# Kernel optimization log

Hardware: AMD Instinct MI355X
Metric: run time of the kernel (lower is better)

The kernel has to match this reference:

```python
import jax, jax.numpy as jnp
import numpy as np

EPS = 1e-5


def setup_inputs() -> dict:
    key = jax.random.key(0)
    ks = jax.random.split(key, 5)
    N, E, D, L = 10000, 160000, 512, 3
    x = jax.random.normal(ks[0], (N, D), dtype=jnp.float32)
    src = jax.random.randint(ks[1], (E,), 0, N, dtype=jnp.int64)
    dst = jax.random.randint(ks[2], (E,), 0, N, dtype=jnp.int64)
    gamma = jnp.ones((L, D), dtype=jnp.float32)
    beta = jnp.zeros((L, D), dtype=jnp.float32)
    # glorot-ish scale so ReLU stack stays well-conditioned
    W = jax.random.normal(ks[3], (L, D, D), dtype=jnp.float32) * (1.0 / np.sqrt(D))
    b = jnp.zeros((L, D), dtype=jnp.float32)
    return {"x": x, "src": src, "dst": dst, "gamma": gamma, "beta": beta, "W": W, "b": b}


def reference(x, src, dst, gamma, beta, W, b):
    N = x.shape[0]
    ones = jnp.ones(src.shape[0], dtype=x.dtype)
    # DGL GraphConv norm='both': src side uses out-degree, dst side uses in-degree
    out_deg = jnp.clip(jax.ops.segment_sum(ones, src, num_segments=N), 1.0)
    in_deg = jnp.clip(jax.ops.segment_sum(ones, dst, num_segments=N), 1.0)
    src_norm = (out_deg ** -0.5)[:, None]  # [N,1]
    dst_norm = (in_deg ** -0.5)[:, None]   # [N,1]
    n_layers = gamma.shape[0]
    for i in range(n_layers):
        # BatchNorm1d (training mode: batch mean, biased variance)
        mu = jnp.mean(x, axis=0)
        var = jnp.var(x, axis=0)
        x = (x - mu) * jax.lax.rsqrt(var + EPS) * gamma[i] + beta[i]
        h = x * src_norm
        agg = jax.ops.segment_sum(h[src], dst, num_segments=N) * dst_norm
        x = jax.nn.relu(agg @ W[i] + b[i])
    return x
```

## Files before the change

kernel.cpp:

```cpp
#include <hip/hip_runtime.h>
#include <hip/hip_bf16.h>

constexpr int N = 10000;
constexpr int D = 512;
constexpr int E = 160000;
constexpr int L = 3;
constexpr float EPS = 1e-5f;

typedef _Float16 half8 __attribute__((ext_vector_type(8)));
typedef _Float16 half2v __attribute__((ext_vector_type(2)));
typedef float floatx4 __attribute__((ext_vector_type(4)));

__device__ __forceinline__ void glds16(const _Float16* g, _Float16* l) {
    __builtin_amdgcn_global_load_lds(
        (const __attribute__((address_space(1))) uint32_t*)(g),
        (__attribute__((address_space(3))) uint32_t*)(l),
        16, 0, 0);
}

constexpr int DEG_BLOCKS  = (E + 255) / 256;
constexpr int CONV_BLOCKS = 100;
constexpr int TW_BLOCKS   = L * 256;
constexpr int MEGA_BLOCKS = DEG_BLOCKS + CONV_BLOCKS + TW_BLOCKS;

__global__ __launch_bounds__(256) void mega_setup(
    const int* __restrict__ src, const int* __restrict__ dst,
    const float* __restrict__ x, const float* __restrict__ W,
    int* __restrict__ out_deg, int* __restrict__ in_deg,
    _Float16* __restrict__ x16, float* __restrict__ stats0,
    _Float16* __restrict__ Wt) {
    __shared__ float tb[32][33];
    int bid = blockIdx.x;
    int tid = threadIdx.x;
    if (bid < DEG_BLOCKS) {
        int e = bid * 256 + tid;
        if (e < E) {
            atomicAdd(&out_deg[src[e]], 1);
            atomicAdd(&in_deg[dst[e]], 1);
        }
    } else if (bid < DEG_BLOCKS + CONV_BLOCKS) {
        int b = bid - DEG_BLOCKS;
        int r0 = b * 100;
        int r1 = r0 + 100; if (r1 > N) r1 = N;
        int c2 = tid * 2;
        float s0 = 0.f, s1 = 0.f, q0 = 0.f, q1 = 0.f;
        for (int r = r0; r < r1; ++r) {
            float2 v = *(const float2*)(x + (size_t)r * D + c2);
            s0 += v.x; q0 += v.x * v.x;
            s1 += v.y; q1 += v.y * v.y;
            half2v h; h[0] = (_Float16)v.x; h[1] = (_Float16)v.y;
            *(half2v*)(x16 + (size_t)r * D + c2) = h;
        }
        atomicAdd(&stats0[c2], s0);
        atomicAdd(&stats0[c2 + 1], s1);
        atomicAdd(&stats0[D + c2], q0);
        atomicAdd(&stats0[D + c2 + 1], q1);
    } else {
        int b = bid - DEG_BLOCKS - CONV_BLOCKS;
        int l = b >> 8;
        int t = b & 255;
        int k0 = (t >> 4) * 32, n0 = (t & 15) * 32;
        int tx = tid & 31, ty = tid >> 5;
        const float* Wl = W + (size_t)l * D * D;
        _Float16* Wtl = Wt + (size_t)l * D * D;
        for (int i = 0; i < 32; i += 8)
            tb[ty + i][tx] = Wl[(size_t)(k0 + ty + i) * D + n0 + tx];
        __syncthreads();
        for (int i = 0; i < 32; i += 8)
            Wtl[(size_t)(n0 + ty + i) * D + k0 + tx] = (_Float16)tb[tx][ty + i];
    }
}

__global__ void scan_indeg(const int* __restrict__ in_deg,
                           const int* __restrict__ out_deg,
                           int* __restrict__ off, int* __restrict__ cursor,
                           float* __restrict__ src_norm, float* __restrict__ dst_norm) {
    __shared__ int lsum[1024];
    int t = threadIdx.x;
    const int chunk = (N + 1023) / 1024;
    int start = t * chunk;
    int end = start + chunk; if (end > N) end = N;
    int s = 0;
    for (int i = start; i < end; ++i) s += in_deg[i];
    lsum[t] = s;
    __syncthreads();
    for (int d = 1; d < 1024; d <<= 1) {
        int v = (t >= d) ? lsum[t - d] : 0;
        __syncthreads();
        lsum[t] += v;
        __syncthreads();
    }
    int excl = (t == 0) ? 0 : lsum[t - 1];
    for (int i = start; i < end; ++i) {
        off[i] = excl;
        cursor[i] = excl;
        excl += in_deg[i];
        int od = out_deg[i]; if (od < 1) od = 1;
        int id = in_deg[i];  if (id < 1) id = 1;
        src_norm[i] = rsqrtf((float)od);
        dst_norm[i] = rsqrtf((float)id);
    }
    if (t == 1023) off[N] = lsum[1023];
}

__global__ void csr_fill(const int* __restrict__ src, const int* __restrict__ dst,
                         int* __restrict__ cursor, int* __restrict__ csr_src) {
    int e = blockIdx.x * blockDim.x + threadIdx.x;
    if (e >= E) return;
    int d = dst[e];
    int pos = atomicAdd(&cursor[d], 1);
    csr_src[pos] = src[e];
}

__global__ __launch_bounds__(256) void aggregate_bn(
    const _Float16* __restrict__ x, const int* __restrict__ off,
    const int* __restrict__ csr_src, const float* __restrict__ src_norm,
    const float* __restrict__ dst_norm, const float* __restrict__ stats,
    const float* __restrict__ gamma, const float* __restrict__ beta,
    _Float16* __restrict__ agg) {
    int wid = (blockIdx.x * 256 + threadIdx.x) >> 6;
    if (wid >= N) return;
    int lane = threadIdx.x & 63;
    int c0 = lane * 8;

    float scale[8], shift[8];
    const float invN = 1.0f / (float)N;
    for (int i = 0; i < 8; ++i) {
        int c = c0 + i;
        float mu = stats[c] * invN;
        float var = stats[D + c] * invN - mu * mu;
        float sc = gamma[c] * rsqrtf(var + EPS);
        scale[i] = sc;
        shift[i] = beta[c] - mu * sc;
    }

    int e0 = off[wid], e1 = off[wid + 1];
    float a[8] = {}, a2[8] = {};
    float t = 0.f;
    int e = e0;
    for (; e + 4 <= e1; e += 4) {
        int s0 = csr_src[e];
        int s1 = csr_src[e + 1];
        int s2 = csr_src[e + 2];
        int s3 = csr_src[e + 3];
        float n0 = src_norm[s0];
        float n1 = src_norm[s1];
        float n2 = src_norm[s2];
        float n3 = src_norm[s3];
        half8 v0 = *(const half8*)(x + (size_t)s0 * D + c0);
        half8 v1 = *(const half8*)(x + (size_t)s1 * D + c0);
        half8 v2 = *(const half8*)(x + (size_t)s2 * D + c0);
        half8 v3 = *(const half8*)(x + (size_t)s3 * D + c0);
        t += (n0 + n1) + (n2 + n3);
        for (int k = 0; k < 8; ++k) {
            a[k]  += (float)v0[k] * n0;
            a2[k] += (float)v1[k] * n1;
            a[k]  += (float)v2[k] * n2;
            a2[k] += (float)v3[k] * n3;
        }
    }
    for (; e < e1; ++e) {
        int s0 = csr_src[e];
        float n0 = src_norm[s0];
        half8 v0 = *(const half8*)(x + (size_t)s0 * D + c0);
        t += n0;
        for (int k = 0; k < 8; ++k) a[k] += (float)v0[k] * n0;
    }
    float dn = dst_norm[wid];
    half8 o;
    for (int i = 0; i < 8; ++i)
        o[i] = (_Float16)(dn * (scale[i] * (a[i] + a2[i]) + shift[i] * t));
    *(half8*)(agg + (size_t)wid * D + c0) = o;
}

template <typename OutT, bool STATS>
__global__ __launch_bounds__(256) void mm_f16_relu(
    const _Float16* __restrict__ A, const _Float16* __restrict__ Bt,
    const float* __restrict__ bias, OutT* __restrict__ C, int M,
    float* __restrict__ stats) {
    __shared__ __align__(16) _Float16 As[128 * 32];
    __shared__ __align__(16) _Float16 Bs[128 * 32];
    const int tid  = threadIdx.x;
    const int wave = tid >> 6;
    const int lane = tid & 63;
    const int quad = lane >> 4;
    const int l16  = lane & 15;
    const int row0 = blockIdx.x * 128;
    const int col0 = blockIdx.y * 128;
    const int wm = (wave & 1) * 64;
    const int wn = (wave >> 1) * 64;
    const int sr = lane >> 2;
    const int sc = (lane & 3) * 8;

    int ar0 = row0 + wave * 32 + sr;
    int ar1 = ar0 + 16;
    if (ar0 >= M) ar0 = M - 1;
    if (ar1 >= M) ar1 = M - 1;
    const _Float16* gA0 = A + (size_t)ar0 * D + sc;
    const _Float16* gA1 = A + (size_t)ar1 * D + sc;
    const _Float16* gB0 = Bt + (size_t)(col0 + wave * 32 + sr) * D + sc;
    const _Float16* gB1 = Bt + (size_t)(col0 + wave * 32 + 16 + sr) * D + sc;
    _Float16* lA0 = As + (wave * 32) * 32;
    _Float16* lA1 = As + (wave * 32 + 16) * 32;
    _Float16* lB0 = Bs + (wave * 32) * 32;
    _Float16* lB1 = Bs + (wave * 32 + 16) * 32;

    floatx4 acc[4][4] = {};

    for (int k0 = 0; k0 < D; k0 += 32) {
        __syncthreads();
        glds16(gA0 + k0, lA0);
        glds16(gA1 + k0, lA1);
        glds16(gB0 + k0, lB0);
        glds16(gB1 + k0, lB1);
        __syncthreads();
        half8 af[4], bf[4];
        for (int i = 0; i < 4; ++i)
            af[i] = *(const half8*)(As + (wm + i * 16 + l16) * 32 + quad * 8);
        for (int j = 0; j < 4; ++j)
            bf[j] = *(const half8*)(Bs + (wn + j * 16 + l16) * 32 + quad * 8);
        for (int i = 0; i < 4; ++i)
            for (int j = 0; j < 4; ++j)
                acc[i][j] = __builtin_amdgcn_mfma_f32_16x16x32_f16(
                    af[i], bf[j], acc[i][j], 0, 0, 0);
    }

    float s[4] = {}, q[4] = {};
    for (int i = 0; i < 4; ++i) {
        for (int r = 0; r < 4; ++r) {
            int row = row0 + wm + i * 16 + quad * 4 + r;
            bool valid = row < M;
            for (int j = 0; j < 4; ++j) {
                int col = col0 + wn + j * 16 + l16;
                float v = acc[i][j][r] + bias[col];
                v = v > 0.f ? v : 0.f;
                if (valid) {
                    C[(size_t)row * D + col] = (OutT)v;
                    if (STATS) { s[j] += v; q[j] += v * v; }
                }
            }
        }
    }
    if (STATS) {
        for (int j = 0; j < 4; ++j) {
            float sv = s[j], qv = q[j];
            sv += __shfl_xor(sv, 16); sv += __shfl_xor(sv, 32);
            qv += __shfl_xor(qv, 16); qv += __shfl_xor(qv, 32);
            if (quad == 0) {
                int col = col0 + wn + j * 16 + l16;
                atomicAdd(&stats[col], sv);
                atomicAdd(&stats[D + col], qv);
            }
        }
    }
}

extern "C" void kernel_launch(void* const* d_in, const int* in_sizes, int n_in,
                              void* d_out, int out_size, void* d_ws, size_t ws_size,
                              hipStream_t stream) {
    const float* x_in  = (const float*)d_in[0];
    const int*   src   = (const int*)d_in[1];
    const int*   dst   = (const int*)d_in[2];
    const float* gamma = (const float*)d_in[3];
    const float* beta  = (const float*)d_in[4];
    const float* W     = (const float*)d_in[5];
    const float* b     = (const float*)d_in[6];
    float* out = (float*)d_out;

    char* p = (char*)d_ws;
    _Float16* x16 = (_Float16*)p;  p += (size_t)N * D * 2;
    _Float16* agg = (_Float16*)p;  p += (size_t)N * D * 2;
    _Float16* Wt  = (_Float16*)p;  p += (size_t)L * D * D * 2;
    float* src_norm = (float*)p;   p += (size_t)N * 4;
    float* dst_norm = (float*)p;   p += (size_t)N * 4;
    int* out_deg   = (int*)p;      p += (size_t)N * 4;
    int* in_deg    = (int*)p;      p += (size_t)N * 4;
    float* stats0  = (float*)p;    p += 2 * D * 4;
    float* stats1  = (float*)p;    p += 2 * D * 4;
    float* stats2  = (float*)p;    p += 2 * D * 4;
    int* csr_off   = (int*)p;      p += (size_t)(N + 1) * 4;
    int* cursor    = (int*)p;      p += (size_t)N * 4;
    int* csr_src   = (int*)p;      p += (size_t)E * 4;

    float* stats_in[3] = {stats0, stats1, stats2};

    hipMemsetAsync(out_deg, 0, (2 * (size_t)N + 6 * D) * sizeof(int), stream);
    mega_setup<<<MEGA_BLOCKS, 256, 0, stream>>>(src, dst, x_in, W,
                                                out_deg, in_deg, x16, stats0, Wt);
    scan_indeg<<<1, 1024, 0, stream>>>(in_deg, out_deg, csr_off, cursor,
                                       src_norm, dst_norm);
    csr_fill<<<DEG_BLOCKS, 256, 0, stream>>>(src, dst, cursor, csr_src);

    dim3 mm_grid((N + 127) / 128, D / 128);
    const int agg_blocks = (N + 3) / 4;

    for (int l = 0; l < L; ++l) {
        const float* gl  = gamma + (size_t)l * D;
        const float* bl  = beta + (size_t)l * D;
        const _Float16* Wl = Wt + (size_t)l * D * D;
        const float* bil = b + (size_t)l * D;

        aggregate_bn<<<agg_blocks, 256, 0, stream>>>(
            x16, csr_off, csr_src, src_norm, dst_norm, stats_in[l], gl, bl, agg);
        if (l == L - 1) {
            mm_f16_relu<float, false><<<mm_grid, 256, 0, stream>>>(
                agg, Wl, bil, out, N, nullptr);
        } else {
            mm_f16_relu<_Float16, true><<<mm_grid, 256, 0, stream>>>(
                agg, Wl, bil, x16, N, stats_in[l + 1]);
        }
    }
}
```

Before: 281.4 us.

## Store activations in column-chunked layout to shrink gather working set

Feature activations and aggregation outputs are stored as four column chunks of 128 halves each ([chunk][N][128]) instead of row-major [N][512]. The aggregation kernel now assigns each block to one chunk and eight nodes, so concurrently running blocks gather from a smaller slice of memory that fits better in cache. Each lane now reads 4-byte half2 values instead of 16-byte half8 values, which means more, narrower gathers and repeated index and norm loads per chunk. The GEMM A loads and the layer-output stores are updated to use the chunked layout.

```diff
diff --git a/kernel.cpp b/kernel.cpp
--- a/kernel.cpp
+++ b/kernel.cpp
@@ -6,6 +6,8 @@
 constexpr int E = 160000;
 constexpr int L = 3;
 constexpr float EPS = 1e-5f;
+constexpr int CHUNK = 128;
+constexpr int NCH = D / CHUNK;
 
 typedef _Float16 half8 __attribute__((ext_vector_type(8)));
 typedef _Float16 half2v __attribute__((ext_vector_type(2)));
@@ -43,13 +45,16 @@
         int r0 = b * 100;
         int r1 = r0 + 100; if (r1 > N) r1 = N;
         int c2 = tid * 2;
+        int ch = c2 >> 7;
+        int lc = c2 & 127;
+        _Float16* xc = x16 + (size_t)ch * N * CHUNK;
         float s0 = 0.f, s1 = 0.f, q0 = 0.f, q1 = 0.f;
         for (int r = r0; r < r1; ++r) {
             float2 v = *(const float2*)(x + (size_t)r * D + c2);
             s0 += v.x; q0 += v.x * v.x;
             s1 += v.y; q1 += v.y * v.y;
             half2v h; h[0] = (_Float16)v.x; h[1] = (_Float16)v.y;
-            *(half2v*)(x16 + (size_t)r * D + c2) = h;
+            *(half2v*)(xc + (size_t)r * CHUNK + lc) = h;
         }
         atomicAdd(&stats0[c2], s0);
         atomicAdd(&stats0[c2 + 1], s1);
@@ -118,15 +123,24 @@
     const float* __restrict__ dst_norm, const float* __restrict__ stats,
     const float* __restrict__ gamma, const float* __restrict__ beta,
     _Float16* __restrict__ agg) {
-    int wid = (blockIdx.x * 256 + threadIdx.x) >> 6;
-    if (wid >= N) return;
+    int bid = blockIdx.x;
+    int g = bid >> 3;
+    int xx = bid & 7;
+    int ch = xx >> 1;
+    int sub = xx & 1;
+    int wave = threadIdx.x >> 6;
     int lane = threadIdx.x & 63;
-    int c0 = lane * 8;
-
-    float scale[8], shift[8];
+    int n = g * 8 + sub * 4 + wave;
+    int lc = lane * 2;
+    int gc = ch * CHUNK + lc;
+
+    const _Float16* xc = x + (size_t)ch * N * CHUNK;
+    _Float16* ac = agg + (size_t)ch * N * CHUNK;
+
+    float scale[2], shift[2];
     const float invN = 1.0f / (float)N;
-    for (int i = 0; i < 8; ++i) {
-        int c = c0 + i;
+    for (int i = 0; i < 2; ++i) {
+        int c = gc + i;
         float mu = stats[c] * invN;
         float var = stats[D + c] * invN - mu * mu;
         float sc = gamma[c] * rsqrtf(var + EPS);
@@ -134,8 +148,8 @@
         shift[i] = beta[c] - mu * sc;
     }
 
-    int e0 = off[wid], e1 = off[wid + 1];
-    float a[8] = {}, a2[8] = {};
+    int e0 = off[n], e1 = off[n + 1];
+    float a[2] = {}, a2[2] = {};
     float t = 0.f;
     int e = e0;
     for (; e + 4 <= e1; e += 4) {
@@ -147,30 +161,28 @@
         float n1 = src_norm[s1];
         float n2 = src_norm[s2];
         float n3 = src_norm[s3];
-        half8 v0 = *(const half8*)(x + (size_t)s0 * D + c0);
-        half8 v1 = *(const half8*)(x + (size_t)s1 * D + c0);
-        half8 v2 = *(const half8*)(x + (size_t)s2 * D + c0);
-        half8 v3 = *(const half8*)(x + (size_t)s3 * D + c0);
+        half2v v0 = *(const half2v*)(xc + (size_t)s0 * CHUNK + lc);
+        half2v v1 = *(const half2v*)(xc + (size_t)s1 * CHUNK + lc);
+        half2v v2 = *(const half2v*)(xc + (size_t)s2 * CHUNK + lc);
+        half2v v3 = *(const half2v*)(xc + (size_t)s3 * CHUNK + lc);
         t += (n0 + n1) + (n2 + n3);
-        for (int k = 0; k < 8; ++k) {
-            a[k]  += (float)v0[k] * n0;
-            a2[k] += (float)v1[k] * n1;
-            a[k]  += (float)v2[k] * n2;
-            a2[k] += (float)v3[k] * n3;
+        for (int k = 0; k < 2; ++k) {
+            a[k]  += (float)v0[k] * n0 + (float)v2[k] * n2;
+            a2[k] += (float)v1[k] * n1 + (float)v3[k] * n3;
         }
     }
     for (; e < e1; ++e) {
         int s0 = csr_src[e];
         float n0 = src_norm[s0];
-        half8 v0 = *(const half8*)(x + (size_t)s0 * D + c0);
+        half2v v0 = *(const half2v*)(xc + (size_t)s0 * CHUNK + lc);
         t += n0;
-        for (int k = 0; k < 8; ++k) a[k] += (float)v0[k] * n0;
-    }
-    float dn = dst_norm[wid];
-    half8 o;
-    for (int i = 0; i < 8; ++i)
+        for (int k = 0; k < 2; ++k) a[k] += (float)v0[k] * n0;
+    }
+    float dn = dst_norm[n];
+    half2v o;
+    for (int i = 0; i < 2; ++i)
         o[i] = (_Float16)(dn * (scale[i] * (a[i] + a2[i]) + shift[i] * t));
-    *(half8*)(agg + (size_t)wid * D + c0) = o;
+    *(half2v*)(ac + (size_t)n * CHUNK + lc) = o;
 }
 
 template <typename OutT, bool STATS>
@@ -196,8 +208,8 @@
     int ar1 = ar0 + 16;
     if (ar0 >= M) ar0 = M - 1;
     if (ar1 >= M) ar1 = M - 1;
-    const _Float16* gA0 = A + (size_t)ar0 * D + sc;
-    const _Float16* gA1 = A + (size_t)ar1 * D + sc;
+    const size_t aoff0 = (size_t)ar0 * CHUNK + sc;
+    const size_t aoff1 = (size_t)ar1 * CHUNK + sc;
     const _Float16* gB0 = Bt + (size_t)(col0 + wave * 32 + sr) * D + sc;
     const _Float16* gB1 = Bt + (size_t)(col0 + wave * 32 + 16 + sr) * D + sc;
     _Float16* lA0 = As + (wave * 32) * 32;
@@ -208,9 +220,10 @@
     floatx4 acc[4][4] = {};
 
     for (int k0 = 0; k0 < D; k0 += 32) {
-        __syncthreads();
-        glds16(gA0 + k0, lA0);
-        glds16(gA1 + k0, lA1);
+        const _Float16* Ac = A + (size_t)(k0 >> 7) * M * CHUNK + (k0 & 127);
+        __syncthreads();
+        glds16(Ac + aoff0, lA0);
+        glds16(Ac + aoff1, lA1);
         glds16(gB0 + k0, lB0);
         glds16(gB1 + k0, lB1);
         __syncthreads();
@@ -225,18 +238,23 @@
                     af[i], bf[j], acc[i][j], 0, 0, 0);
     }
 
+    _Float16* Cc = (_Float16*)C + (size_t)(col0 >> 7) * M * CHUNK;
     float s[4] = {}, q[4] = {};
     for (int i = 0; i < 4; ++i) {
         for (int r = 0; r < 4; ++r) {
             int row = row0 + wm + i * 16 + quad * 4 + r;
             bool valid = row < M;
             for (int j = 0; j < 4; ++j) {
-                int col = col0 + wn + j * 16 + l16;
-                float v = acc[i][j][r] + bias[col];
+                int lcol = wn + j * 16 + l16;
+                float v = acc[i][j][r] + bias[col0 + lcol];
                 v = v > 0.f ? v : 0.f;
                 if (valid) {
-                    C[(size_t)row * D + col] = (OutT)v;
-                    if (STATS) { s[j] += v; q[j] += v * v; }
+                    if (STATS) {
+                        Cc[(size_t)row * CHUNK + lcol] = (_Float16)v;
+                        s[j] += v; q[j] += v * v;
+                    } else {
+                        C[(size_t)row * D + col0 + lcol] = (OutT)v;
+                    }
                 }
             }
         }
@@ -292,7 +310,7 @@
     csr_fill<<<DEG_BLOCKS, 256, 0, stream>>>(src, dst, cursor, csr_src);
 
     dim3 mm_grid((N + 127) / 128, D / 128);
-    const int agg_blocks = (N + 3) / 4;
+    const int agg_blocks = (N / 8) * 8;
 
     for (int l = 0; l < L; ++l) {
         const float* gl  = gamma + (size_t)l * D;
```

After: 296.6 us. +5.4%, slower.

## Split node features into two column-chunk planes for cache-friendlier gather

Applied to the files above, without the earlier changes.

Stores the fp16 node features as two planes of 256 columns each ([2][N][256]) instead of row-major [N][512]. The aggregation kernel runs twice as many blocks, each covering one column half with 4-wide loads, so each plane (about 5 MB) is more likely to stay in cache during the random neighbor gather. The GEMM epilogue and the setup conversion write into the chunked layout. In exchange, index and CSR loads are repeated per chunk and vector loads get narrower.

```diff
diff --git a/kernel.cpp b/kernel.cpp
--- a/kernel.cpp
+++ b/kernel.cpp
@@ -6,8 +6,10 @@
 constexpr int E = 160000;
 constexpr int L = 3;
 constexpr float EPS = 1e-5f;
+constexpr int CH = 256;
 
 typedef _Float16 half8 __attribute__((ext_vector_type(8)));
+typedef _Float16 half4v __attribute__((ext_vector_type(4)));
 typedef _Float16 half2v __attribute__((ext_vector_type(2)));
 typedef float floatx4 __attribute__((ext_vector_type(4)));
 
@@ -43,13 +45,16 @@
         int r0 = b * 100;
         int r1 = r0 + 100; if (r1 > N) r1 = N;
         int c2 = tid * 2;
+        int ch = c2 >> 8;
+        int lc = c2 & 255;
+        _Float16* xc = x16 + (size_t)ch * N * CH;
         float s0 = 0.f, s1 = 0.f, q0 = 0.f, q1 = 0.f;
         for (int r = r0; r < r1; ++r) {
             float2 v = *(const float2*)(x + (size_t)r * D + c2);
             s0 += v.x; q0 += v.x * v.x;
             s1 += v.y; q1 += v.y * v.y;
             half2v h; h[0] = (_Float16)v.x; h[1] = (_Float16)v.y;
-            *(half2v*)(x16 + (size_t)r * D + c2) = h;
+            *(half2v*)(xc + (size_t)r * CH + lc) = h;
         }
         atomicAdd(&stats0[c2], s0);
         atomicAdd(&stats0[c2 + 1], s1);
@@ -118,15 +123,21 @@
     const float* __restrict__ dst_norm, const float* __restrict__ stats,
     const float* __restrict__ gamma, const float* __restrict__ beta,
     _Float16* __restrict__ agg) {
-    int wid = (blockIdx.x * 256 + threadIdx.x) >> 6;
-    if (wid >= N) return;
+    int bid = blockIdx.x;
+    int ch = bid >= 2500;
+    int bb = ch ? bid - 2500 : bid;
+    int wave = threadIdx.x >> 6;
     int lane = threadIdx.x & 63;
-    int c0 = lane * 8;
-
-    float scale[8], shift[8];
+    int n = bb * 4 + wave;
+    int lc = lane * 4;
+    int gc = ch * CH + lc;
+
+    const _Float16* xc = x + (size_t)ch * N * CH;
+
+    float scale[4], shift[4];
     const float invN = 1.0f / (float)N;
-    for (int i = 0; i < 8; ++i) {
-        int c = c0 + i;
+    for (int i = 0; i < 4; ++i) {
+        int c = gc + i;
         float mu = stats[c] * invN;
         float var = stats[D + c] * invN - mu * mu;
         float sc = gamma[c] * rsqrtf(var + EPS);
@@ -134,8 +145,8 @@
         shift[i] = beta[c] - mu * sc;
     }
 
-    int e0 = off[wid], e1 = off[wid + 1];
-    float a[8] = {}, a2[8] = {};
+    int e0 = off[n], e1 = off[n + 1];
+    float a[4] = {}, a2[4] = {};
     float t = 0.f;
     int e = e0;
     for (; e + 4 <= e1; e += 4) {
@@ -147,12 +158,12 @@
         float n1 = src_norm[s1];
         float n2 = src_norm[s2];
         float n3 = src_norm[s3];
-        half8 v0 = *(const half8*)(x + (size_t)s0 * D + c0);
-        half8 v1 = *(const half8*)(x + (size_t)s1 * D + c0);
-        half8 v2 = *(const half8*)(x + (size_t)s2 * D + c0);
-        half8 v3 = *(const half8*)(x + (size_t)s3 * D + c0);
+        half4v v0 = *(const half4v*)(xc + (size_t)s0 * CH + lc);
+        half4v v1 = *(const half4v*)(xc + (size_t)s1 * CH + lc);
+        half4v v2 = *(const half4v*)(xc + (size_t)s2 * CH + lc);
+        half4v v3 = *(const half4v*)(xc + (size_t)s3 * CH + lc);
         t += (n0 + n1) + (n2 + n3);
-        for (int k = 0; k < 8; ++k) {
+        for (int k = 0; k < 4; ++k) {
             a[k]  += (float)v0[k] * n0;
             a2[k] += (float)v1[k] * n1;
             a[k]  += (float)v2[k] * n2;
@@ -162,15 +173,15 @@
     for (; e < e1; ++e) {
         int s0 = csr_src[e];
         float n0 = src_norm[s0];
-        half8 v0 = *(const half8*)(x + (size_t)s0 * D + c0);
+        half4v v0 = *(const half4v*)(xc + (size_t)s0 * CH + lc);
         t += n0;
-        for (int k = 0; k < 8; ++k) a[k] += (float)v0[k] * n0;
-    }
-    float dn = dst_norm[wid];
-    half8 o;
-    for (int i = 0; i < 8; ++i)
+        for (int k = 0; k < 4; ++k) a[k] += (float)v0[k] * n0;
+    }
+    float dn = dst_norm[n];
+    half4v o;
+    for (int i = 0; i < 4; ++i)
         o[i] = (_Float16)(dn * (scale[i] * (a[i] + a2[i]) + shift[i] * t));
-    *(half8*)(agg + (size_t)wid * D + c0) = o;
+    *(half4v*)(agg + (size_t)n * D + gc) = o;
 }
 
 template <typename OutT, bool STATS>
@@ -225,6 +236,7 @@
                     af[i], bf[j], acc[i][j], 0, 0, 0);
     }
 
+    _Float16* Cc = (_Float16*)C + (size_t)(col0 >> 8) * M * CH;
     float s[4] = {}, q[4] = {};
     for (int i = 0; i < 4; ++i) {
         for (int r = 0; r < 4; ++r) {
@@ -235,8 +247,12 @@
                 float v = acc[i][j][r] + bias[col];
                 v = v > 0.f ? v : 0.f;
                 if (valid) {
-                    C[(size_t)row * D + col] = (OutT)v;
-                    if (STATS) { s[j] += v; q[j] += v * v; }
+                    if (STATS) {
+                        Cc[(size_t)row * CH + (col & 255)] = (_Float16)v;
+                        s[j] += v; q[j] += v * v;
+                    } else {
+                        C[(size_t)row * D + col] = (OutT)v;
+                    }
                 }
             }
         }
@@ -292,7 +308,7 @@
     csr_fill<<<DEG_BLOCKS, 256, 0, stream>>>(src, dst, cursor, csr_src);
 
     dim3 mm_grid((N + 127) / 128, D / 128);
-    const int agg_blocks = (N + 3) / 4;
+    const int agg_blocks = 5000;
 
     for (int l = 0; l < L; ++l) {
         const float* gl  = gamma + (size_t)l * D;
```

Measured after the change: 283.5 us. About the same (+0.8%).

## Merge aggregation and GEMM per layer with row-block flags; fuse scan and CSR fill

Applied to the files above, without the earlier changes.

Each layer now launches a single kernel. The first blocks do the gather-aggregate with BatchNorm and bump a per-128-row-block counter, and the later GEMM blocks spin on that counter before loading their A tile. The point is to overlap the GEMM of finished row blocks with the aggregation still running and to cut launch gaps. The degree scan and CSR fill are likewise merged into one kernel, with a release/acquire flag written by block 0. Two ping-pong x buffers are used because the GEMM output would otherwise overwrite the input that aggregation blocks are still reading. The scheme depends on blocks being dispatched in order, so spinning blocks cannot starve the producers, and it adds busy-wait overhead.

```diff
diff --git a/kernel.cpp b/kernel.cpp
--- a/kernel.cpp
+++ b/kernel.cpp
@@ -71,122 +71,155 @@
     }
 }
 
-__global__ void scan_indeg(const int* __restrict__ in_deg,
-                           const int* __restrict__ out_deg,
-                           int* __restrict__ off, int* __restrict__ cursor,
-                           float* __restrict__ src_norm, float* __restrict__ dst_norm) {
-    __shared__ int lsum[1024];
-    int t = threadIdx.x;
-    const int chunk = (N + 1023) / 1024;
-    int start = t * chunk;
-    int end = start + chunk; if (end > N) end = N;
-    int s = 0;
-    for (int i = start; i < end; ++i) s += in_deg[i];
-    lsum[t] = s;
-    __syncthreads();
-    for (int d = 1; d < 1024; d <<= 1) {
-        int v = (t >= d) ? lsum[t - d] : 0;
-        __syncthreads();
-        lsum[t] += v;
-        __syncthreads();
-    }
-    int excl = (t == 0) ? 0 : lsum[t - 1];
-    for (int i = start; i < end; ++i) {
-        off[i] = excl;
-        cursor[i] = excl;
-        excl += in_deg[i];
-        int od = out_deg[i]; if (od < 1) od = 1;
-        int id = in_deg[i];  if (id < 1) id = 1;
-        src_norm[i] = rsqrtf((float)od);
-        dst_norm[i] = rsqrtf((float)id);
-    }
-    if (t == 1023) off[N] = lsum[1023];
-}
-
-__global__ void csr_fill(const int* __restrict__ src, const int* __restrict__ dst,
-                         int* __restrict__ cursor, int* __restrict__ csr_src) {
-    int e = blockIdx.x * blockDim.x + threadIdx.x;
-    if (e >= E) return;
-    int d = dst[e];
-    int pos = atomicAdd(&cursor[d], 1);
-    csr_src[pos] = src[e];
-}
-
-__global__ __launch_bounds__(256) void aggregate_bn(
-    const _Float16* __restrict__ x, const int* __restrict__ off,
+__global__ __launch_bounds__(256) void scan_fill(
+    const int* __restrict__ in_deg, const int* __restrict__ out_deg,
+    int* __restrict__ off, int* __restrict__ cursor,
+    float* __restrict__ src_norm, float* __restrict__ dst_norm,
+    const int* __restrict__ src, const int* __restrict__ dst,
+    int* __restrict__ csr_src, int* flag) {
+    if (blockIdx.x == 0) {
+        __shared__ int lsum[256];
+        int t = threadIdx.x;
+        const int chunk = (N + 255) / 256;
+        int start = t * chunk;
+        int end = start + chunk; if (end > N) end = N;
+        int s = 0;
+        for (int i = start; i < end; ++i) s += in_deg[i];
+        lsum[t] = s;
+        __syncthreads();
+        for (int d = 1; d < 256; d <<= 1) {
+            int v = (t >= d) ? lsum[t - d] : 0;
+            __syncthreads();
+            lsum[t] += v;
+            __syncthreads();
+        }
+        int excl = (t == 0) ? 0 : lsum[t - 1];
+        for (int i = start; i < end; ++i) {
+            off[i] = excl;
+            cursor[i] = excl;
+            excl += in_deg[i];
+            int od = out_deg[i]; if (od < 1) od = 1;
+            int id = in_deg[i];  if (id < 1) id = 1;
+            src_norm[i] = rsqrtf((float)od);
+            dst_norm[i] = rsqrtf((float)id);
+        }
+        if (t == 255) off[N] = lsum[255];
+        __syncthreads();
+        if (t == 0)
+            __hip_atomic_store(flag, 1, __ATOMIC_RELEASE, __HIP_MEMORY_SCOPE_AGENT);
+    } else {
+        if (threadIdx.x == 0) {
+            while (!__hip_atomic_load(flag, __ATOMIC_RELAXED, __HIP_MEMORY_SCOPE_AGENT))
+                __builtin_amdgcn_s_sleep(8);
+            (void)__hip_atomic_load(flag, __ATOMIC_ACQUIRE, __HIP_MEMORY_SCOPE_AGENT);
+        }
+        __syncthreads();
+        __builtin_amdgcn_fence(__ATOMIC_ACQUIRE, "agent");
+        int e = (blockIdx.x - 1) * 256 + threadIdx.x;
+        if (e < E) {
+            int d_ = dst[e];
+            int pos = atomicAdd(&cursor[d_], 1);
+            csr_src[pos] = src[e];
+        }
+    }
+}
+
+constexpr int AGG_BLOCKS = N / 4;
+constexpr int MM_RB = (N + 127) / 128;
+constexpr int MM_CB = D / 128;
+constexpr int MM_BLOCKS = MM_RB * MM_CB;
+
+template <typename OutT, bool STATS>
+__global__ __launch_bounds__(256) void layer_merged(
+    const _Float16* __restrict__ xin, const int* __restrict__ off,
     const int* __restrict__ csr_src, const float* __restrict__ src_norm,
-    const float* __restrict__ dst_norm, const float* __restrict__ stats,
+    const float* __restrict__ dst_norm, const float* __restrict__ stats_in,
     const float* __restrict__ gamma, const float* __restrict__ beta,
-    _Float16* __restrict__ agg) {
-    int wid = (blockIdx.x * 256 + threadIdx.x) >> 6;
-    if (wid >= N) return;
-    int lane = threadIdx.x & 63;
-    int c0 = lane * 8;
-
-    float scale[8], shift[8];
-    const float invN = 1.0f / (float)N;
-    for (int i = 0; i < 8; ++i) {
-        int c = c0 + i;
-        float mu = stats[c] * invN;
-        float var = stats[D + c] * invN - mu * mu;
-        float sc = gamma[c] * rsqrtf(var + EPS);
-        scale[i] = sc;
-        shift[i] = beta[c] - mu * sc;
-    }
-
-    int e0 = off[wid], e1 = off[wid + 1];
-    float a[8] = {}, a2[8] = {};
-    float t = 0.f;
-    int e = e0;
-    for (; e + 4 <= e1; e += 4) {
-        int s0 = csr_src[e];
-        int s1 = csr_src[e + 1];
-        int s2 = csr_src[e + 2];
-        int s3 = csr_src[e + 3];
-        float n0 = src_norm[s0];
-        float n1 = src_norm[s1];
-        float n2 = src_norm[s2];
-        float n3 = src_norm[s3];
-        half8 v0 = *(const half8*)(x + (size_t)s0 * D + c0);
-        half8 v1 = *(const half8*)(x + (size_t)s1 * D + c0);
-        half8 v2 = *(const half8*)(x + (size_t)s2 * D + c0);
-        half8 v3 = *(const half8*)(x + (size_t)s3 * D + c0);
-        t += (n0 + n1) + (n2 + n3);
-        for (int k = 0; k < 8; ++k) {
-            a[k]  += (float)v0[k] * n0;
-            a2[k] += (float)v1[k] * n1;
-            a[k]  += (float)v2[k] * n2;
-            a2[k] += (float)v3[k] * n3;
-        }
-    }
-    for (; e < e1; ++e) {
-        int s0 = csr_src[e];
-        float n0 = src_norm[s0];
-        half8 v0 = *(const half8*)(x + (size_t)s0 * D + c0);
-        t += n0;
-        for (int k = 0; k < 8; ++k) a[k] += (float)v0[k] * n0;
-    }
-    float dn = dst_norm[wid];
-    half8 o;
-    for (int i = 0; i < 8; ++i)
-        o[i] = (_Float16)(dn * (scale[i] * (a[i] + a2[i]) + shift[i] * t));
-    *(half8*)(agg + (size_t)wid * D + c0) = o;
-}
-
-template <typename OutT, bool STATS>
-__global__ __launch_bounds__(256) void mm_f16_relu(
-    const _Float16* __restrict__ A, const _Float16* __restrict__ Bt,
-    const float* __restrict__ bias, OutT* __restrict__ C, int M,
-    float* __restrict__ stats) {
+    _Float16* __restrict__ agg, const _Float16* __restrict__ Bt,
+    const float* __restrict__ bias, OutT* __restrict__ C,
+    float* __restrict__ stats_out, int* __restrict__ rb_cnt) {
     __shared__ __align__(16) _Float16 As[128 * 32];
     __shared__ __align__(16) _Float16 Bs[128 * 32];
     const int tid  = threadIdx.x;
+    const int bid  = blockIdx.x;
     const int wave = tid >> 6;
     const int lane = tid & 63;
     const int quad = lane >> 4;
     const int l16  = lane & 15;
-    const int row0 = blockIdx.x * 128;
-    const int col0 = blockIdx.y * 128;
+
+    if (bid < AGG_BLOCKS) {
+        int n = bid * 4 + wave;
+        int c0 = lane * 8;
+        float scale[8], shift[8];
+        const float invN = 1.0f / (float)N;
+        for (int i = 0; i < 8; ++i) {
+            int c = c0 + i;
+            float mu = stats_in[c] * invN;
+            float var = stats_in[D + c] * invN - mu * mu;
+            float sc = gamma[c] * rsqrtf(var + EPS);
+            scale[i] = sc;
+            shift[i] = beta[c] - mu * sc;
+        }
+        int e0 = off[n], e1 = off[n + 1];
+        float a[8] = {}, a2[8] = {};
+        float t = 0.f;
+        int e = e0;
+        for (; e + 4 <= e1; e += 4) {
+            int s0 = csr_src[e];
+            int s1 = csr_src[e + 1];
+            int s2 = csr_src[e + 2];
+            int s3 = csr_src[e + 3];
+            float n0 = src_norm[s0];
+            float n1 = src_norm[s1];
+            float n2 = src_norm[s2];
+            float n3 = src_norm[s3];
+            half8 v0 = *(const half8*)(xin + (size_t)s0 * D + c0);
+            half8 v1 = *(const half8*)(xin + (size_t)s1 * D + c0);
+            half8 v2 = *(const half8*)(xin + (size_t)s2 * D + c0);
+            half8 v3 = *(const half8*)(xin + (size_t)s3 * D + c0);
+            t += (n0 + n1) + (n2 + n3);
+            for (int k = 0; k < 8; ++k) {
+                a[k]  += (float)v0[k] * n0;
+                a2[k] += (float)v1[k] * n1;
+                a[k]  += (float)v2[k] * n2;
+                a2[k] += (float)v3[k] * n3;
+            }
+        }
+        for (; e < e1; ++e) {
+            int s0 = csr_src[e];
+            float n0 = src_norm[s0];
+            half8 v0 = *(const half8*)(xin + (size_t)s0 * D + c0);
+            t += n0;
+            for (int k = 0; k < 8; ++k) a[k] += (float)v0[k] * n0;
+        }
+        float dn = dst_norm[n];
+        half8 o;
+        for (int i = 0; i < 8; ++i)
+            o[i] = (_Float16)(dn * (scale[i] * (a[i] + a2[i]) + shift[i] * t));
+        *(half8*)(agg + (size_t)n * D + c0) = o;
+        __syncthreads();
+        if (tid == 0)
+            __hip_atomic_fetch_add(&rb_cnt[bid >> 5], 1, __ATOMIC_RELEASE,
+                                   __HIP_MEMORY_SCOPE_AGENT);
+        return;
+    }
+
+    const int idx = bid - AGG_BLOCKS;
+    const int rb = idx % MM_RB;
+    const int cb = idx / MM_RB;
+    if (tid == 0) {
+        const int target = (rb < N / 128) ? 32 : (N / 4 - (N / 128) * 32);
+        while (__hip_atomic_load(&rb_cnt[rb], __ATOMIC_RELAXED,
+                                 __HIP_MEMORY_SCOPE_AGENT) < target)
+            __builtin_amdgcn_s_sleep(8);
+        (void)__hip_atomic_load(&rb_cnt[rb], __ATOMIC_ACQUIRE,
+                                __HIP_MEMORY_SCOPE_AGENT);
+    }
+    __syncthreads();
+    __builtin_amdgcn_fence(__ATOMIC_ACQUIRE, "agent");
+
+    const int row0 = rb * 128;
+    const int col0 = cb * 128;
     const int wm = (wave & 1) * 64;
     const int wn = (wave >> 1) * 64;
     const int sr = lane >> 2;
@@ -194,10 +227,10 @@
 
     int ar0 = row0 + wave * 32 + sr;
     int ar1 = ar0 + 16;
-    if (ar0 >= M) ar0 = M - 1;
-    if (ar1 >= M) ar1 = M - 1;
-    const _Float16* gA0 = A + (size_t)ar0 * D + sc;
-    const _Float16* gA1 = A + (size_t)ar1 * D + sc;
+    if (ar0 >= N) ar0 = N - 1;
+    if (ar1 >= N) ar1 = N - 1;
+    const _Float16* gA0 = agg + (size_t)ar0 * D + sc;
+    const _Float16* gA1 = agg + (size_t)ar1 * D + sc;
     const _Float16* gB0 = Bt + (size_t)(col0 + wave * 32 + sr) * D + sc;
     const _Float16* gB1 = Bt + (size_t)(col0 + wave * 32 + 16 + sr) * D + sc;
     _Float16* lA0 = As + (wave * 32) * 32;
@@ -229,7 +262,7 @@
     for (int i = 0; i < 4; ++i) {
         for (int r = 0; r < 4; ++r) {
             int row = row0 + wm + i * 16 + quad * 4 + r;
-            bool valid = row < M;
+            bool valid = row < N;
             for (int j = 0; j < 4; ++j) {
                 int col = col0 + wn + j * 16 + l16;
                 float v = acc[i][j][r] + bias[col];
@@ -248,8 +281,8 @@
             qv += __shfl_xor(qv, 16); qv += __shfl_xor(qv, 32);
             if (quad == 0) {
                 int col = col0 + wn + j * 16 + l16;
-                atomicAdd(&stats[col], sv);
-                atomicAdd(&stats[D + col], qv);
+                atomicAdd(&stats_out[col], sv);
+                atomicAdd(&stats_out[D + col], qv);
             }
         }
     }
@@ -268,9 +301,10 @@
     float* out = (float*)d_out;
 
     char* p = (char*)d_ws;
-    _Float16* x16 = (_Float16*)p;  p += (size_t)N * D * 2;
-    _Float16* agg = (_Float16*)p;  p += (size_t)N * D * 2;
-    _Float16* Wt  = (_Float16*)p;  p += (size_t)L * D * D * 2;
+    _Float16* x16a = (_Float16*)p; p += (size_t)N * D * 2;
+    _Float16* x16b = (_Float16*)p; p += (size_t)N * D * 2;
+    _Float16* agg  = (_Float16*)p; p += (size_t)N * D * 2;
+    _Float16* Wt   = (_Float16*)p; p += (size_t)L * D * D * 2;
     float* src_norm = (float*)p;   p += (size_t)N * 4;
     float* dst_norm = (float*)p;   p += (size_t)N * 4;
     int* out_deg   = (int*)p;      p += (size_t)N * 4;
@@ -278,36 +312,29 @@
     float* stats0  = (float*)p;    p += 2 * D * 4;
     float* stats1  = (float*)p;    p += 2 * D * 4;
     float* stats2  = (float*)p;    p += 2 * D * 4;
+    int* flag      = (int*)p;      p += 16 * 4;
+    int* rb_cnt    = (int*)p;      p += 3 * 128 * 4;
+    size_t zero_bytes = (size_t)((char*)p - (char*)out_deg);
     int* csr_off   = (int*)p;      p += (size_t)(N + 1) * 4;
     int* cursor    = (int*)p;      p += (size_t)N * 4;
     int* csr_src   = (int*)p;      p += (size_t)E * 4;
 
-    float* stats_in[3] = {stats0, stats1, stats2};
-
-    hipMemsetAsync(out_deg, 0, (2 * (size_t)N + 6 * D) * sizeof(int), stream);
+    hipMemsetAsync(out_deg, 0, zero_bytes, stream);
     mega_setup<<<MEGA_BLOCKS, 256, 0, stream>>>(src, dst, x_in, W,
-                                                out_deg, in_deg, x16, stats0, Wt);
-    scan_indeg<<<1, 1024, 0, stream>>>(in_deg, out_deg, csr_off, cursor,
-                                       src_norm, dst_norm);
-    csr_fill<<<DEG_BLOCKS, 256, 0, stream>>>(src, dst, cursor, csr_src);
-
-    dim3 mm_grid((N + 127) / 128, D / 128);
-    const int agg_blocks = (N + 3) / 4;
-
-    for (int l = 0; l < L; ++l) {
-        const float* gl  = gamma + (size_t)l * D;
-        const float* bl  = beta + (size_t)l * D;
-        const _Float16* Wl = Wt + (size_t)l * D * D;
-        const float* bil = b + (size_t)l * D;
-
-        aggregate_bn<<<agg_blocks, 256, 0, stream>>>(
-            x16, csr_off, csr_src, src_norm, dst_norm, stats_in[l], gl, bl, agg);
-        if (l == L - 1) {
-            mm_f16_relu<float, false><<<mm_grid, 256, 0, stream>>>(
-                agg, Wl, bil, out, N, nullptr);
-        } else {
-            mm_f16_relu<_Float16, true><<<mm_grid, 256, 0, stream>>>(
-                agg, Wl, bil, x16, N, stats_in[l + 1]);
-        }
-    }
-}
+                                                out_deg, in_deg, x16a, stats0, Wt);
+    scan_fill<<<1 + DEG_BLOCKS, 256, 0, stream>>>(in_deg, out_deg, csr_off, cursor,
+                                                  src_norm, dst_norm, src, dst,
+                                                  csr_src, flag);
+
+    const int grid = AGG_BLOCKS + MM_BLOCKS;
+
+    layer_merged<_Float16, true><<<grid, 256, 0, stream>>>(
+        x16a, csr_off, csr_src, src_norm, dst_norm, stats0, gamma, beta,
+        agg, Wt, b, x16b, stats1, rb_cnt);
+    layer_merged<_Float16, true><<<grid, 256, 0, stream>>>(
+        x16b, csr_off, csr_src, src_norm, dst_norm, stats1, gamma + D, beta + D,
+        agg, Wt + (size_t)D * D, b + D, x16a, stats2, rb_cnt + 128);
+    layer_merged<float, false><<<grid, 256, 0, stream>>>(
+        x16a, csr_off, csr_src, src_norm, dst_norm, stats2, gamma + 2 * D, beta + 2 * D,
+        agg, Wt + 2 * (size_t)D * D, b + 2 * D, out, nullptr, rb_cnt + 256);
+}
```

Result: slower. 620.6 us (+120.6%).
